# Performance work log

Hardware: AMD Instinct MI355X
Metric: run time of the kernel (lower is better)

The kernel has to match this reference:

```python
import jax, jax.numpy as jnp
import numpy as np

FOCAL_ALPHA = 0.25
FOCAL_GAMMA = 2.0
W_MASK = 20.0   # weight_dict['loss_mask'], used only for best-mask selection
W_DICE = 1.0    # weight_dict['loss_dice']
DIV_WEIGHT = 0.001
DIV_THRESHOLD = 0.5
DIV_EPS = 1e-5


def setup_inputs() -> dict:
    key = jax.random.key(0)
    k1, k2, k3 = jax.random.split(key, 3)
    T, N, M, H, W = 8, 4, 3, 512, 512
    pred_masks = jax.random.normal(k1, (T, N, M, H, W), dtype=jnp.float32) * 2.0
    pred_ious = jax.random.uniform(k2, (T, N, M), dtype=jnp.float32)
    targets = (jax.random.uniform(k3, (T, N, H, W)) > 0.7).astype(jnp.float32)
    return {"pred_masks": pred_masks, "pred_ious": pred_ious, "targets": targets}


def _diversity_loss(preds, tgts):
    # preds, tgts: [N, M, P] (flattened pixels). Returns [N].
    cond = (preds.max() > 1.0) | (preds.min() < 0.0)
    probs = jnp.where(cond, jax.nn.sigmoid(preds), preds)
    target_region = (tgts > 0.5).any(axis=1)            # [N, P]
    m = probs > DIV_THRESHOLD                            # [N, M, P]
    pair_pred = m[:, :, None, :] | m[:, None, :, :]      # [N, M, M, P]
    active = (pair_pred & target_region[:, None, None, :]).astype(probs.dtype)
    inter = jnp.einsum('nip,njp,nijp->nij', probs, probs, active)
    s = jnp.einsum('nip,nijp->nij', probs, active)
    union = s + jnp.swapaxes(s, 1, 2) - inter + DIV_EPS  # active is symmetric in (i,j)
    overlap = inter / union                              # 0 when no active pixels (0/eps)
    Mc = probs.shape[1]
    triu = jnp.triu(jnp.ones((Mc, Mc), probs.dtype), k=1)
    num_pairs = Mc * (Mc - 1) / 2
    return (overlap * triu[None]).sum(axis=(1, 2)) / (num_pairs + DIV_EPS)


def _frame_losses(src, ious, tgt, num_objects):
    # src: [N, M, H, W] logits, ious: [N, M], tgt: [N, H, W] binary
    N, M, H, W = src.shape
    P = H * W
    sf = src.reshape(N, M, P)
    tf = jnp.broadcast_to(tgt[:, None], src.shape).reshape(N, M, P)
    prob = jax.nn.sigmoid(sf)
    # stable BCE-with-logits
    ce = jnp.maximum(sf, 0.0) - sf * tf + jnp.log1p(jnp.exp(-jnp.abs(sf)))
    p_t = prob * tf + (1.0 - prob) * (1.0 - tf)
    fl = ce * (1.0 - p_t) ** FOCAL_GAMMA
    alpha_t = FOCAL_ALPHA * tf + (1.0 - FOCAL_ALPHA) * (1.0 - tf)
    fl = alpha_t * fl
    focal = fl.mean(-1) / num_objects                    # [N, M]
    div = _diversity_loss(sf, tf)                        # [N]
    loss_multimask = focal + DIV_WEIGHT * div[:, None]   # [N, M]
    # dice (on sigmoid probs)
    numer = 2.0 * (prob * tf).sum(-1)
    denom = prob.sum(-1) + tf.sum(-1)
    loss_multidice = (1.0 - (numer + 1.0) / (denom + 1.0)) / num_objects  # [N, M]
    # iou (MSE between predicted and actual binary IoU)
    pm = sf > 0
    gm = tf > 0
    area_i = (pm & gm).sum(-1).astype(sf.dtype)
    area_u = (pm | gm).sum(-1).astype(sf.dtype)
    actual_ious = area_i / jnp.maximum(area_u, 1.0)
    loss_multiiou = (ious - actual_ious) ** 2 / num_objects  # [N, M]
    # pick best mask channel per object by weighted mask+dice loss
    combo = W_MASK * loss_multimask + W_DICE * loss_multidice
    best = jnp.argmin(combo, axis=-1)
    rows = jnp.arange(N)
    return jnp.stack([
        loss_multimask[rows, best].sum(),
        loss_multidice[rows, best].sum(),
        loss_multiiou[rows, best].sum(),
    ])


def reference(pred_masks, pred_ious, targets):
    # pred_masks: [T, N, M, H, W]; pred_ious: [T, N, M]; targets: [T, N, H, W]
    num_objects = jnp.maximum(jnp.asarray(targets.shape[1], jnp.float32), 1.0)
    per_frame = jax.vmap(lambda s, i, t: _frame_losses(s, i, t, num_objects))(
        pred_masks, pred_ious, targets)           # [T, 3]
    return per_frame.sum(axis=0)                  # [loss_mask, loss_dice, loss_iou]
```

## Files before the change

kernel.cpp:

```cpp
#include <hip/hip_runtime.h>
#include <math.h>

constexpr int Tn = 8, Nn = 4, Mn = 3;
constexpr int Hn = 512, Wn = 512;
constexpr int Pn = Hn * Wn;
constexpr int NTN = Tn * Nn;
constexpr int ACC = 24;
constexpr int TPB = 256;
constexpr int BLOCKS_PER_TN = 64;
constexpr int V4_PER_TN = Pn / 4;
constexpr int V4_PER_BLOCK = V4_PER_TN / BLOCKS_PER_TN;
constexpr int ITERS = V4_PER_BLOCK / TPB;


__device__ __forceinline__ float sig_and_log1pexp(float s, float& L) {
  float a = fabsf(s);
  float e = __expf(-a);
  float r = __builtin_amdgcn_rcpf(1.0f + e);
  L = __logf(1.0f + e);
  return (s >= 0.0f) ? r : e * r;
}

__global__ __launch_bounds__(TPB) void accum_kernel(
    const float* __restrict__ masks,
    const float* __restrict__ targets,
    float* __restrict__ ws) {
  const int tn    = blockIdx.y;
  const int chunk = blockIdx.x;
  const int tid   = threadIdx.x;

  const float4* m0p = (const float4*)(masks + ((size_t)tn * Mn + 0) * Pn);
  const float4* m1p = (const float4*)(masks + ((size_t)tn * Mn + 1) * Pn);
  const float4* m2p = (const float4*)(masks + ((size_t)tn * Mn + 2) * Pn);
  const float4* tp  = (const float4*)(targets + (size_t)tn * Pn);

  float acc[22];
#pragma unroll
  for (int i = 0; i < 22; ++i) acc[i] = 0.0f;

#pragma unroll
  for (int it = 0; it < ITERS; ++it) {
    const int v = chunk * V4_PER_BLOCK + it * TPB + tid;
    float4 a0 = m0p[v];
    float4 a1 = m1p[v];
    float4 a2 = m2p[v];
    float4 tt = tp[v];
    const float sv0[4] = {a0.x, a0.y, a0.z, a0.w};
    const float sv1[4] = {a1.x, a1.y, a1.z, a1.w};
    const float sv2[4] = {a2.x, a2.y, a2.z, a2.w};
    const float tv[4]  = {tt.x, tt.y, tt.z, tt.w};

#pragma unroll
    for (int j = 0; j < 4; ++j) {
      const float t  = tv[j];
      const bool  gm = t > 0.5f;
      float L0, L1, L2;
      const float q0 = sig_and_log1pexp(sv0[j], L0);
      const float q1 = sig_and_log1pexp(sv1[j], L1);
      const float q2 = sig_and_log1pexp(sv2[j], L2);
      const float qs[3] = {q0, q1, q2};
      const float Ls[3] = {L0, L1, L2};
      const float ss[3] = {sv0[j], sv1[j], sv2[j]};

#pragma unroll
      for (int m = 0; m < 3; ++m) {
        const float s = ss[m], q = qs[m], L = Ls[m];
        const float ce  = fmaxf(s, 0.0f) - s * t + L;
        const float omp = gm ? (1.0f - q) : q;
        const float at  = gm ? 0.25f : 0.75f;
        acc[0 + m] += at * ce * omp * omp;
        acc[3 + m] += q * t;
        acc[6 + m] += q;
        const bool pm = s > 0.0f;
        acc[9 + m]  += (pm && gm) ? 1.0f : 0.0f;
        acc[12 + m] += (pm || gm) ? 1.0f : 0.0f;
      }
      acc[15] += t;

      const bool b0 = ss[0] > 0.0f, b1 = ss[1] > 0.0f, b2 = ss[2] > 0.0f;
      const float w01 = (gm && (b0 | b1)) ? 1.0f : 0.0f;
      const float w02 = (gm && (b0 | b2)) ? 1.0f : 0.0f;
      const float w12 = (gm && (b1 | b2)) ? 1.0f : 0.0f;
      acc[16] += w01 * (q0 * q1);
      acc[17] += w02 * (q0 * q2);
      acc[18] += w12 * (q1 * q2);
      acc[19] += w01 * (q0 + q1);
      acc[20] += w02 * (q0 + q2);
      acc[21] += w12 * (q1 + q2);
    }
  }

  __shared__ float red[TPB / 64][22];
  const int lane = tid & 63, wave = tid >> 6;
#pragma unroll
  for (int i = 0; i < 22; ++i) {
    float v = acc[i];
#pragma unroll
    for (int off = 32; off > 0; off >>= 1) v += __shfl_down(v, off);
    if (lane == 0) red[wave][i] = v;
  }
  __syncthreads();
  if (tid < 22) {
    float v = red[0][tid] + red[1][tid] + red[2][tid] + red[3][tid];
    atomicAdd(&ws[tn * ACC + tid], v);
  }
}

__global__ __launch_bounds__(64) void finalize_kernel(
    const float* __restrict__ ws,
    const float* __restrict__ ious,
    float* __restrict__ out) {
  const int tid = threadIdx.x;
  float lm = 0.0f, ld = 0.0f, li = 0.0f;
  if (tid < NTN) {
    const float* a = ws + tid * ACC;
    float div = 0.0f;
#pragma unroll
    for (int k = 0; k < 3; ++k) {
      const float inter = a[16 + k];
      const float uni   = a[19 + k] - inter + 1e-5f;
      div += inter / uni;
    }
    div /= (3.0f + 1e-5f);

    const float invP  = 1.0f / (float)Pn;
    const float invNo = 1.0f / (float)Nn;
    float bc = 1e30f;
#pragma unroll
    for (int m = 0; m < 3; ++m) {
      const float focal = a[m] * invP * invNo;
      const float lmask = focal + 0.001f * div;
      const float dice  = (1.0f - (2.0f * a[3 + m] + 1.0f) /
                                  (a[6 + m] + a[15] + 1.0f)) * invNo;
      const float aiou  = a[9 + m] / fmaxf(a[12 + m], 1.0f);
      const float pi    = ious[tid * 3 + m];
      const float liou  = (pi - aiou) * (pi - aiou) * invNo;
      const float combo = 20.0f * lmask + dice;
      if (combo < bc) { bc = combo; lm = lmask; ld = dice; li = liou; }
    }
  }
#pragma unroll
  for (int off = 32; off > 0; off >>= 1) {
    lm += __shfl_down(lm, off);
    ld += __shfl_down(ld, off);
    li += __shfl_down(li, off);
  }
  if (tid == 0) { out[0] = lm; out[1] = ld; out[2] = li; }
}

extern "C" void kernel_launch(void* const* d_in, const int* in_sizes, int n_in,
                              void* d_out, int out_size, void* d_ws, size_t ws_size,
                              hipStream_t stream) {
  const float* masks   = (const float*)d_in[0];
  const float* ious    = (const float*)d_in[1];
  const float* targets = (const float*)d_in[2];
  float* out = (float*)d_out;
  float* ws  = (float*)d_ws;

  hipMemsetAsync(ws, 0, NTN * ACC * sizeof(float), stream);

  dim3 grid(BLOCKS_PER_TN, NTN);
  accum_kernel<<<grid, TPB, 0, stream>>>(masks, targets, ws);
  finalize_kernel<<<1, 64, 0, stream>>>(ws, ious, out);
}
```

Before: 191.8 us.

## Simplify per-pixel loss math to branchless FMAs and prefetch next loads

Rewrites the per-pixel math to use sigmoid via exp(-s) and log(1+exp(-s)) directly, with arithmetic blends in place of select branches. Union is now derived from a pred-positive count plus the target sum. Also software-prefetches the next iteration's float4 loads into registers. The aim is fewer VALU instructions per pixel and better latency hiding, at the cost of more live registers and possible overflow of exp(-s) for very negative logits.

```diff
diff --git a/kernel.cpp b/kernel.cpp
--- a/kernel.cpp
+++ b/kernel.cpp
@@ -13,12 +13,23 @@
 constexpr int ITERS = V4_PER_BLOCK / TPB;
 
 
-__device__ __forceinline__ float sig_and_log1pexp(float s, float& L) {
-  float a = fabsf(s);
-  float e = __expf(-a);
-  float r = __builtin_amdgcn_rcpf(1.0f + e);
-  L = __logf(1.0f + e);
-  return (s >= 0.0f) ? r : e * r;
+
+__device__ __forceinline__ void pixel_update(
+    const float s, const float t, const float omt, const float at,
+    float& aF, float& aQT, float& aQ, float& aI, float& aP,
+    float& q, float& fp) {
+  const float u   = __expf(-s);
+  const float d   = 1.0f + u;
+  q               = __builtin_amdgcn_rcpf(d);
+  const float lnd = __logf(d);
+  const float ce  = __builtin_fmaf(s, omt, lnd);
+  const float omp = __builtin_fmaf(t, __builtin_fmaf(-2.0f, q, 1.0f), q);
+  aF  = __builtin_fmaf(at * ce, omp * omp, aF);
+  aQT = __builtin_fmaf(q, t, aQT);
+  aQ += q;
+  fp  = (s > 0.0f) ? 1.0f : 0.0f;
+  aI  = __builtin_fmaf(fp, t, aI);
+  aP += fp;
 }
 
 __global__ __launch_bounds__(TPB) void accum_kernel(
@@ -33,75 +44,77 @@
   const float4* m1p = (const float4*)(masks + ((size_t)tn * Mn + 1) * Pn);
   const float4* m2p = (const float4*)(masks + ((size_t)tn * Mn + 2) * Pn);
   const float4* tp  = (const float4*)(targets + (size_t)tn * Pn);
+  const int vbase = chunk * V4_PER_BLOCK + tid;
 
-  float acc[22];
-#pragma unroll
-  for (int i = 0; i < 22; ++i) acc[i] = 0.0f;
+  float aF0 = 0.f, aF1 = 0.f, aF2 = 0.f;
+  float aQT0 = 0.f, aQT1 = 0.f, aQT2 = 0.f;
+  float aQ0 = 0.f, aQ1 = 0.f, aQ2 = 0.f;
+  float aI0 = 0.f, aI1 = 0.f, aI2 = 0.f;
+  float aP0 = 0.f, aP1 = 0.f, aP2 = 0.f;
+  float aT = 0.f;
+  float aPI0 = 0.f, aPI1 = 0.f, aPI2 = 0.f;
+  float aPS0 = 0.f, aPS1 = 0.f, aPS2 = 0.f;
+
+  float4 nA0 = m0p[vbase];
+  float4 nA1 = m1p[vbase];
+  float4 nA2 = m2p[vbase];
+  float4 nT  = tp[vbase];
 
 #pragma unroll
   for (int it = 0; it < ITERS; ++it) {
-    const int v = chunk * V4_PER_BLOCK + it * TPB + tid;
-    float4 a0 = m0p[v];
-    float4 a1 = m1p[v];
-    float4 a2 = m2p[v];
-    float4 tt = tp[v];
-    const float sv0[4] = {a0.x, a0.y, a0.z, a0.w};
-    const float sv1[4] = {a1.x, a1.y, a1.z, a1.w};
-    const float sv2[4] = {a2.x, a2.y, a2.z, a2.w};
-    const float tv[4]  = {tt.x, tt.y, tt.z, tt.w};
+    const float4 cA0 = nA0, cA1 = nA1, cA2 = nA2, cT = nT;
+    if (it + 1 < ITERS) {
+      const int v = vbase + (it + 1) * TPB;
+      nA0 = m0p[v];
+      nA1 = m1p[v];
+      nA2 = m2p[v];
+      nT  = tp[v];
+    }
+
+    const float sv0[4] = {cA0.x, cA0.y, cA0.z, cA0.w};
+    const float sv1[4] = {cA1.x, cA1.y, cA1.z, cA1.w};
+    const float sv2[4] = {cA2.x, cA2.y, cA2.z, cA2.w};
+    const float tv[4]  = {cT.x, cT.y, cT.z, cT.w};
 
 #pragma unroll
     for (int j = 0; j < 4; ++j) {
-      const float t  = tv[j];
-      const bool  gm = t > 0.5f;
-      float L0, L1, L2;
-      const float q0 = sig_and_log1pexp(sv0[j], L0);
-      const float q1 = sig_and_log1pexp(sv1[j], L1);
-      const float q2 = sig_and_log1pexp(sv2[j], L2);
-      const float qs[3] = {q0, q1, q2};
-      const float Ls[3] = {L0, L1, L2};
-      const float ss[3] = {sv0[j], sv1[j], sv2[j]};
+      const float t   = tv[j];
+      const float omt = 1.0f - t;
+      const float at  = __builtin_fmaf(t, -0.5f, 0.75f);
 
-#pragma unroll
-      for (int m = 0; m < 3; ++m) {
-        const float s = ss[m], q = qs[m], L = Ls[m];
-        const float ce  = fmaxf(s, 0.0f) - s * t + L;
-        const float omp = gm ? (1.0f - q) : q;
-        const float at  = gm ? 0.25f : 0.75f;
-        acc[0 + m] += at * ce * omp * omp;
-        acc[3 + m] += q * t;
-        acc[6 + m] += q;
-        const bool pm = s > 0.0f;
-        acc[9 + m]  += (pm && gm) ? 1.0f : 0.0f;
-        acc[12 + m] += (pm || gm) ? 1.0f : 0.0f;
-      }
-      acc[15] += t;
+      float q0, q1, q2, fp0, fp1, fp2;
+      pixel_update(sv0[j], t, omt, at, aF0, aQT0, aQ0, aI0, aP0, q0, fp0);
+      pixel_update(sv1[j], t, omt, at, aF1, aQT1, aQ1, aI1, aP1, q1, fp1);
+      pixel_update(sv2[j], t, omt, at, aF2, aQT2, aQ2, aI2, aP2, q2, fp2);
+      aT += t;
 
-      const bool b0 = ss[0] > 0.0f, b1 = ss[1] > 0.0f, b2 = ss[2] > 0.0f;
-      const float w01 = (gm && (b0 | b1)) ? 1.0f : 0.0f;
-      const float w02 = (gm && (b0 | b2)) ? 1.0f : 0.0f;
-      const float w12 = (gm && (b1 | b2)) ? 1.0f : 0.0f;
-      acc[16] += w01 * (q0 * q1);
-      acc[17] += w02 * (q0 * q2);
-      acc[18] += w12 * (q1 * q2);
-      acc[19] += w01 * (q0 + q1);
-      acc[20] += w02 * (q0 + q2);
-      acc[21] += w12 * (q1 + q2);
+      const float w01 = fmaxf(fp0, fp1) * t;
+      const float w02 = fmaxf(fp0, fp2) * t;
+      const float w12 = fmaxf(fp1, fp2) * t;
+      aPI0 = __builtin_fmaf(w01, q0 * q1, aPI0);
+      aPI1 = __builtin_fmaf(w02, q0 * q2, aPI1);
+      aPI2 = __builtin_fmaf(w12, q1 * q2, aPI2);
+      aPS0 = __builtin_fmaf(w01, q0 + q1, aPS0);
+      aPS1 = __builtin_fmaf(w02, q0 + q2, aPS1);
+      aPS2 = __builtin_fmaf(w12, q1 + q2, aPS2);
     }
   }
 
+  float accv[22] = {aF0, aF1, aF2, aQT0, aQT1, aQT2, aQ0, aQ1, aQ2,
+                    aI0, aI1, aI2, aP0, aP1, aP2, aT,
+                    aPI0, aPI1, aPI2, aPS0, aPS1, aPS2};
   __shared__ float red[TPB / 64][22];
   const int lane = tid & 63, wave = tid >> 6;
 #pragma unroll
   for (int i = 0; i < 22; ++i) {
-    float v = acc[i];
+    float v = accv[i];
 #pragma unroll
     for (int off = 32; off > 0; off >>= 1) v += __shfl_down(v, off);
     if (lane == 0) red[wave][i] = v;
   }
   __syncthreads();
   if (tid < 22) {
-    float v = red[0][tid] + red[1][tid] + red[2][tid] + red[3][tid];
+    const float v = red[0][tid] + red[1][tid] + red[2][tid] + red[3][tid];
     atomicAdd(&ws[tn * ACC + tid], v);
   }
 }
@@ -111,7 +124,7 @@
     const float* __restrict__ ious,
     float* __restrict__ out) {
   const int tid = threadIdx.x;
-  float lm = 0.0f, ld = 0.0f, li = 0.0f;
+  float lm = 0.f, ld = 0.f, li = 0.f;
   if (tid < NTN) {
     const float* a = ws + tid * ACC;
     float div = 0.0f;
@@ -125,14 +138,16 @@
 
     const float invP  = 1.0f / (float)Pn;
     const float invNo = 1.0f / (float)Nn;
+    const float sumT  = a[15];
     float bc = 1e30f;
 #pragma unroll
     for (int m = 0; m < 3; ++m) {
       const float focal = a[m] * invP * invNo;
       const float lmask = focal + 0.001f * div;
       const float dice  = (1.0f - (2.0f * a[3 + m] + 1.0f) /
-                                  (a[6 + m] + a[15] + 1.0f)) * invNo;
-      const float aiou  = a[9 + m] / fmaxf(a[12 + m], 1.0f);
+                                  (a[6 + m] + sumT + 1.0f)) * invNo;
+      const float uni   = a[12 + m] + sumT - a[9 + m];
+      const float aiou  = a[9 + m] / fmaxf(uni, 1.0f);
       const float pi    = ious[tid * 3 + m];
       const float liou  = (pi - aiou) * (pi - aiou) * invNo;
       const float combo = 20.0f * lmask + dice;
```

New measurement: 183.8 us. 4.2% less time.
